# Optimization experiments

Hardware: AMD Instinct MI355X
Metric: run time of the kernel (lower is better)

Reference implementation:

```python
import jax, jax.numpy as jnp
import numpy as np

BH, BW = 64, 64            # base model input (block) size
STRIDE = 16                # block // 4, per WindowObjectDetector.predict
N_CLASSES = 10
THRESH = 0.7


def _extract_patches(x, bh, bw, stride):
    # x: [1, H, W, 3] -> [R, C, bh, bw, 3], VALID padding (tf.image.extract_patches)
    H, W = x.shape[1], x.shape[2]
    R = (H - bh) // stride + 1
    C = (W - bw) // stride + 1
    r = (jnp.arange(R) * stride)[:, None] + jnp.arange(bh)   # [R, bh]
    c = (jnp.arange(C) * stride)[:, None] + jnp.arange(bw)   # [C, bw]
    p = x[0][r]                 # [R, bh, W, 3]
    p = p[:, :, c]              # [R, bh, C, bw, 3]
    return jnp.transpose(p, (0, 2, 1, 3, 4))  # [R, C, bh, bw, 3]


def _connected_components(mask):
    # mask: bool [K, R, C]; 4-connectivity min-label propagation.
    K, R, C = mask.shape
    BIG = jnp.int32(R * C + 2)
    seed = (jnp.arange(R * C, dtype=jnp.int32).reshape(R, C) + 1)[None]  # [1,R,C]
    lbl0 = jnp.where(mask, seed, 0)

    def prop(l):
        xm = jnp.where(mask, l, BIG)
        n = xm
        n = jnp.minimum(n, jnp.pad(xm, ((0, 0), (1, 0), (0, 0)), constant_values=R * C + 2)[:, :R, :])
        n = jnp.minimum(n, jnp.pad(xm, ((0, 0), (0, 1), (0, 0)), constant_values=R * C + 2)[:, 1:, :])
        n = jnp.minimum(n, jnp.pad(xm, ((0, 0), (0, 0), (1, 0)), constant_values=R * C + 2)[:, :, :C])
        n = jnp.minimum(n, jnp.pad(xm, ((0, 0), (0, 0), (0, 1)), constant_values=R * C + 2)[:, :, 1:])
        return jnp.where(mask, n, 0)

    def cond(carry):
        prev, cur = carry
        return jnp.any(prev != cur)

    def body(carry):
        _, cur = carry
        return cur, prop(cur)

    _, lbl = jax.lax.while_loop(cond, body, (lbl0, prop(lbl0)))
    return lbl  # [K, R, C] int32, 0 = background


def _boxes_from_labels(labels):
    # labels: [K, R, C] -> padded boxes [K, R*C+1, 4] (rowmin-1, colmin-1, rowmax+1, colmax+1)
    K, R, C = labels.shape
    S = R * C + 1
    rr = jnp.repeat(jnp.arange(R, dtype=jnp.int32), C)  # [R*C]
    cc = jnp.tile(jnp.arange(C, dtype=jnp.int32), R)
    flat = labels.reshape(K, R * C)

    def per_class(lbl_k):
        rmin = jax.ops.segment_min(rr, lbl_k, num_segments=S)
        rmax = jax.ops.segment_max(rr, lbl_k, num_segments=S)
        cmin = jax.ops.segment_min(cc, lbl_k, num_segments=S)
        cmax = jax.ops.segment_max(cc, lbl_k, num_segments=S)
        cnt = jax.ops.segment_sum(jnp.ones_like(lbl_k), lbl_k, num_segments=S)
        valid = (cnt > 0) & (jnp.arange(S) > 0)
        box = jnp.stack([rmin - 1, cmin - 1, rmax + 1, cmax + 1], axis=-1)
        box = jnp.where(valid[:, None], box, -1)
        return box, valid

    return jax.vmap(per_class)(flat)


def setup_inputs() -> dict:
    key = jax.random.key(0)
    k1, k2, k3 = jax.random.split(key, 3)
    inputs = jax.random.uniform(k1, (1, 1024, 1024, 3), dtype=jnp.float32)
    W = jax.random.normal(k2, (BH * BW * 3, N_CLASSES), dtype=jnp.float32) * 0.02
    b = jax.random.normal(k3, (N_CLASSES,), dtype=jnp.float32)
    return {"inputs": inputs, "W": W, "b": b}


def reference(inputs, W, b):
    # Windowing: extract 64x64 patches with stride 16 (image divisible by 64 -> no resize)
    patches = _extract_patches(inputs, BH, BW, STRIDE)          # [R, C, 64, 64, 3]
    R, C = patches.shape[0], patches.shape[1]
    flat = patches.reshape(R * C, BH * BW * 3)
    logits = flat @ W + b                                        # base model
    prob = jax.nn.softmax(logits, axis=1).reshape(R, C, N_CLASSES)
    mask = prob > THRESH                                         # [R, C, K]
    # tf transposes before/after connected_components (4-connectivity is symmetric)
    labels = _connected_components(jnp.transpose(mask, (2, 0, 1)))  # [K, R, C]
    labels = jnp.transpose(labels, (1, 2, 0))                    # [R, C, K]
    boxes, valid = _boxes_from_labels(jnp.transpose(labels, (2, 0, 1)))
    return prob, labels, boxes, valid
```

## Files before the change

### kernel.cpp

```cpp
#include <hip/hip_runtime.h>
#include <math.h>

#define RG 61
#define CG 61
#define NP 3721
#define NSEG 3722
#define NCLS 10
#define THRESHV 0.7f
#define BIGI 0x3FFFFFFF

#define NKQ 16
#define NBLK (RG*NKQ)
#define CHS 50
#define ROWF (64*CHS)
#define PROW 610

__global__ __launch_bounds__(256, 3) void wod_logits_part(
    const float* __restrict__ img,
    const float* __restrict__ W,
    float* __restrict__ part)
{
    __shared__ float simg[4 * ROWF];

    const int tid = threadIdx.x;
    const int o  = (blockIdx.x & 7) * 122 + (blockIdx.x >> 3);
    const int r  = o >> 4;
    const int kq = o & 15;
    const int R0 = 16 * r + 4 * kq;

    for (int u = tid; u < 3072; u += 256) {
        const int row = u / 768;
        const int v   = u - row * 768;
        const int p0  = v * 4;
        const float4 x4 = *(const float4*)(img + (size_t)(R0 + row) * 3072 + p0);
        const int ch = p0 / 48;
        const int q  = p0 - ch * 48;
        float* d = simg + row * ROWF + ch * CHS + q;
        *(float2*)d       = make_float2(x4.x, x4.y);
        *(float2*)(d + 2) = make_float2(x4.z, x4.w);
    }
    __syncthreads();

    const int wv = __builtin_amdgcn_readfirstlane(tid >> 6);
    const int c  = tid & 63;
    const int cx = c > 60 ? 60 : c;
    const int wr = 4 * kq + wv;

    const float* wbase = W + wr * 1920;
    const float* srow  = simg + wv * ROWF + cx * CHS;

    float acc[NCLS];
    #pragma unroll
    for (int k = 0; k < NCLS; ++k) acc[k] = 0.f;

    for (int q = 0; q < 24; ++q) {
        #pragma unroll
        for (int j = 0; j < 4; ++j) {
            const int rem = 8 * q + 2 * j;
            const int chq = rem / 48;
            const int uq  = chq * CHS + (rem - 48 * chq);
            const float2 x = *(const float2*)(srow + uq);
            const float* wp = wbase + rem * 10;
            const float4 A0 = *(const float4*)(wp);
            const float4 A1 = *(const float4*)(wp + 4);
            const float4 A2 = *(const float4*)(wp + 8);
            const float4 A3 = *(const float4*)(wp + 12);
            const float4 A4 = *(const float4*)(wp + 16);
            const float w0[NCLS] = {A0.x,A0.y,A0.z,A0.w,A1.x,A1.y,A1.z,A1.w,A2.x,A2.y};
            const float w1[NCLS] = {A2.z,A2.w,A3.x,A3.y,A3.z,A3.w,A4.x,A4.y,A4.z,A4.w};
            #pragma unroll
            for (int k = 0; k < NCLS; ++k) {
                acc[k] = fmaf(x.x, w0[k], acc[k]);
                acc[k] = fmaf(x.y, w1[k], acc[k]);
            }
        }
    }

    if (c < 61) {
        float* pr = part + (size_t)(r * 64 + wr) * PROW + c * 10;
        #pragma unroll
        for (int k = 0; k < NCLS; k += 2)
            *(float2*)(pr + k) = make_float2(acc[k], acc[k + 1]);
    }
}

__global__ __launch_bounds__(256) void wod_reduce(
    const float* __restrict__ part,
    const float* __restrict__ bias,
    float* __restrict__ out_prob,
    int* __restrict__ mask)
{
    __shared__ float lg[PROW];
    const int r   = blockIdx.x;
    const int tid = threadIdx.x;
    const float* pb = part + (size_t)r * 64 * PROW;

    for (int t = tid; t < PROW; t += 256) {
        float s = bias[t - (t / 10) * 10];
        const float* p = pb + t;
        #pragma unroll 8
        for (int wr = 0; wr < 64; ++wr) s += p[wr * PROW];
        lg[t] = s;
    }
    __syncthreads();

    for (int c = tid; c < CG; c += 256) {
        float l[NCLS];
        #pragma unroll
        for (int k = 0; k < NCLS; ++k) l[k] = lg[c * 10 + k];
        float m = -1e30f;
        #pragma unroll
        for (int k = 0; k < NCLS; ++k) m = fmaxf(m, l[k]);
        float ex[NCLS], sm = 0.f;
        #pragma unroll
        for (int k = 0; k < NCLS; ++k) { ex[k] = expf(l[k] - m); sm += ex[k]; }
        const float inv = 1.f / sm;
        const int cell = r * CG + c;
        #pragma unroll
        for (int k = 0; k < NCLS; ++k) {
            const float pr = ex[k] * inv;
            out_prob[cell * 10 + k] = pr;
            mask[k * NP + cell] = (pr > THRESHV) ? 1 : 0;
        }
    }
}

__global__ __launch_bounds__(256) void wod_cc(
    const int* __restrict__ mask,
    float* __restrict__ out_lbl,
    float* __restrict__ out_box,
    float* __restrict__ out_valid)
{
    const int k = blockIdx.x;
    const int tid = threadIdx.x;
    __shared__ int lbl[NP];
    __shared__ int ext0[NSEG], ext1[NSEG];
    __shared__ int changed;

    const int* mk = mask + k * NP;
    for (int idx = tid; idx < NP; idx += 256)
        lbl[idx] = mk[idx] ? (idx + 1) : 0;
    if (tid == 0) changed = 0;
    __syncthreads();

    for (;;) {
        for (int idx = tid; idx < NP; idx += 256) {
            int v = lbl[idx];
            if (v) {
                const int rr = idx / CG;
                const int cc = idx - rr * CG;
                int best = v;
                if (rr > 0)      { int n = lbl[idx - CG]; if (n && n < best) best = n; }
                if (rr < RG - 1) { int n = lbl[idx + CG]; if (n && n < best) best = n; }
                if (cc > 0)      { int n = lbl[idx - 1];  if (n && n < best) best = n; }
                if (cc < CG - 1) { int n = lbl[idx + 1];  if (n && n < best) best = n; }
                if (best < v) { lbl[idx] = best; changed = 1; }
            }
        }
        __syncthreads();
        const bool stop = (changed == 0);
        __syncthreads();
        if (stop) break;
        if (tid == 0) changed = 0;
        __syncthreads();
    }

    for (int idx = tid; idx < NP; idx += 256)
        out_lbl[idx * NCLS + k] = (float)lbl[idx];

    float* boxk = out_box + k * NSEG * 4;
    float* valk = out_valid + k * NSEG;

    for (int s2 = tid; s2 < NSEG; s2 += 256) { ext0[s2] = BIGI; ext1[s2] = BIGI; }
    __syncthreads();
    for (int idx = tid; idx < NP; idx += 256) {
        const int v = lbl[idx];
        if (v) {
            const int rr = idx / CG, cc = idx - rr * CG;
            atomicMin(&ext0[v], rr);
            atomicMin(&ext1[v], cc);
        }
    }
    __syncthreads();
    for (int s2 = tid; s2 < NSEG; s2 += 256) {
        const bool valid = (s2 > 0) && (ext0[s2] != BIGI);
        boxk[s2 * 4 + 0] = valid ? (float)(ext0[s2] - 1) : -1.f;
        boxk[s2 * 4 + 1] = valid ? (float)(ext1[s2] - 1) : -1.f;
        valk[s2] = valid ? 1.f : 0.f;
    }
    __syncthreads();

    for (int s2 = tid; s2 < NSEG; s2 += 256) { ext0[s2] = -1; ext1[s2] = -1; }
    __syncthreads();
    for (int idx = tid; idx < NP; idx += 256) {
        const int v = lbl[idx];
        if (v) {
            const int rr = idx / CG, cc = idx - rr * CG;
            atomicMax(&ext0[v], rr);
            atomicMax(&ext1[v], cc);
        }
    }
    __syncthreads();
    for (int s2 = tid; s2 < NSEG; s2 += 256) {
        const bool valid = (s2 > 0) && (ext0[s2] >= 0);
        boxk[s2 * 4 + 2] = valid ? (float)(ext0[s2] + 1) : -1.f;
        boxk[s2 * 4 + 3] = valid ? (float)(ext1[s2] + 1) : -1.f;
    }
}

extern "C" void kernel_launch(void* const* d_in, const int* in_sizes, int n_in,
                              void* d_out, int out_size, void* d_ws, size_t ws_size,
                              hipStream_t stream) {
    (void)in_sizes; (void)n_in; (void)out_size; (void)ws_size;
    const float* img = (const float*)d_in[0];
    const float* W   = (const float*)d_in[1];
    const float* b   = (const float*)d_in[2];

    float* out       = (float*)d_out;
    float* out_prob  = out;
    float* out_lbl   = out + 37210;
    float* out_box   = out + 74420;
    float* out_valid = out + 223300;

    int*   mask = (int*)d_ws;
    float* part = (float*)((int*)d_ws + NCLS * NP);

    hipLaunchKernelGGL(wod_logits_part, dim3(NBLK), dim3(256), 0, stream,
                       img, W, part);
    hipLaunchKernelGGL(wod_reduce, dim3(RG), dim3(256), 0, stream,
                       part, b, out_prob, mask);
    hipLaunchKernelGGL(wod_cc, dim3(NCLS), dim3(256), 0, stream,
                       mask, out_lbl, out_box, out_valid);
}
```

Measured before the change: 54.30 us.

## Reduce partial sums in-block and load weights via constant address space

Each logits block now sums its four wavefronts' partial logits in shared memory and writes one row instead of four. This cuts partial-sum traffic and the reduce kernel's loop from 64 to 16 terms. Weights are read through an address_space(4) constant pointer so the compiler can use scalar loads, and the loop is restructured per channel. The shared-memory row stride changes to 51 to avoid bank conflicts, at the cost of scalar stores into shared memory and an extra block barrier.

```diff
diff --git a/kernel.cpp b/kernel.cpp
--- a/kernel.cpp
+++ b/kernel.cpp
@@ -11,9 +11,11 @@
 
 #define NKQ 16
 #define NBLK (RG*NKQ)
-#define CHS 50
+#define CHS 51
 #define ROWF (64*CHS)
-#define PROW 610
+#define PROW 640
+
+typedef __attribute__((address_space(4))) const float cfl;
 
 __global__ __launch_bounds__(256, 3) void wod_logits_part(
     const float* __restrict__ img,
@@ -21,7 +23,6 @@
     float* __restrict__ part)
 {
     __shared__ float simg[4 * ROWF];
-
     const int tid = threadIdx.x;
     const int o  = (blockIdx.x & 7) * 122 + (blockIdx.x >> 3);
     const int r  = o >> 4;
@@ -34,10 +35,8 @@
         const int p0  = v * 4;
         const float4 x4 = *(const float4*)(img + (size_t)(R0 + row) * 3072 + p0);
         const int ch = p0 / 48;
-        const int q  = p0 - ch * 48;
-        float* d = simg + row * ROWF + ch * CHS + q;
-        *(float2*)d       = make_float2(x4.x, x4.y);
-        *(float2*)(d + 2) = make_float2(x4.z, x4.w);
+        float* d = simg + row * ROWF + ch * CHS + (p0 - ch * 48);
+        d[0] = x4.x; d[1] = x4.y; d[2] = x4.z; d[3] = x4.w;
     }
     __syncthreads();
 
@@ -46,42 +45,48 @@
     const int cx = c > 60 ? 60 : c;
     const int wr = 4 * kq + wv;
 
-    const float* wbase = W + wr * 1920;
+    const cfl*   wbase = (const cfl*)W + wr * 1920;
     const float* srow  = simg + wv * ROWF + cx * CHS;
 
     float acc[NCLS];
     #pragma unroll
     for (int k = 0; k < NCLS; ++k) acc[k] = 0.f;
 
-    for (int q = 0; q < 24; ++q) {
-        #pragma unroll
-        for (int j = 0; j < 4; ++j) {
-            const int rem = 8 * q + 2 * j;
-            const int chq = rem / 48;
-            const int uq  = chq * CHS + (rem - 48 * chq);
-            const float2 x = *(const float2*)(srow + uq);
-            const float* wp = wbase + rem * 10;
-            const float4 A0 = *(const float4*)(wp);
-            const float4 A1 = *(const float4*)(wp + 4);
-            const float4 A2 = *(const float4*)(wp + 8);
-            const float4 A3 = *(const float4*)(wp + 12);
-            const float4 A4 = *(const float4*)(wp + 16);
-            const float w0[NCLS] = {A0.x,A0.y,A0.z,A0.w,A1.x,A1.y,A1.z,A1.w,A2.x,A2.y};
-            const float w1[NCLS] = {A2.z,A2.w,A3.x,A3.y,A3.z,A3.w,A4.x,A4.y,A4.z,A4.w};
+    #pragma unroll 1
+    for (int cc2 = 0; cc2 < 4; ++cc2) {
+        const float* sch = srow + cc2 * CHS;
+        const cfl*   wch = wbase + cc2 * 480;
+        #pragma unroll
+        for (int q6 = 0; q6 < 6; ++q6) {
             #pragma unroll
-            for (int k = 0; k < NCLS; ++k) {
-                acc[k] = fmaf(x.x, w0[k], acc[k]);
-                acc[k] = fmaf(x.y, w1[k], acc[k]);
+            for (int j = 0; j < 4; ++j) {
+                const int le = q6 * 8 + 2 * j;
+                const float xx = sch[le];
+                const float xy = sch[le + 1];
+                const cfl* wp = wch + le * 10;
+                float w_[20];
+                #pragma unroll
+                for (int k = 0; k < 20; ++k) w_[k] = wp[k];
+                #pragma unroll
+                for (int k = 0; k < NCLS; ++k) {
+                    acc[k] = fmaf(xx, w_[k],      acc[k]);
+                    acc[k] = fmaf(xy, w_[k + 10], acc[k]);
+                }
             }
         }
     }
 
-    if (c < 61) {
-        float* pr = part + (size_t)(r * 64 + wr) * PROW + c * 10;
-        #pragma unroll
-        for (int k = 0; k < NCLS; k += 2)
-            *(float2*)(pr + k) = make_float2(acc[k], acc[k + 1]);
-    }
+    __syncthreads();
+    float* scratch = simg;
+    {
+        float* sc = scratch + wv * PROW + c * 10;
+        #pragma unroll
+        for (int k = 0; k < NCLS; ++k) sc[k] = acc[k];
+    }
+    __syncthreads();
+    for (int t = tid; t < PROW; t += 256)
+        part[(size_t)o * PROW + t] = scratch[t] + scratch[PROW + t]
+                                   + scratch[2 * PROW + t] + scratch[3 * PROW + t];
 }
 
 __global__ __launch_bounds__(256) void wod_reduce(
@@ -93,13 +98,12 @@
     __shared__ float lg[PROW];
     const int r   = blockIdx.x;
     const int tid = threadIdx.x;
-    const float* pb = part + (size_t)r * 64 * PROW;
+    const float* pb = part + (size_t)r * NKQ * PROW;
 
     for (int t = tid; t < PROW; t += 256) {
         float s = bias[t - (t / 10) * 10];
-        const float* p = pb + t;
-        #pragma unroll 8
-        for (int wr = 0; wr < 64; ++wr) s += p[wr * PROW];
+        #pragma unroll 4
+        for (int kq = 0; kq < NKQ; ++kq) s += pb[kq * PROW + t];
         lg[t] = s;
     }
     __syncthreads();
```

Result: faster. 48.35 us (-11.0%).
